# Performance work log

Measured on AMD Instinct MI355X. Metric: run time of the kernel, lower is better.

Reference implementation:

```python
import jax, jax.numpy as jnp
import numpy as np

NHEAD = 8

def setup_inputs() -> dict:
    key = jax.random.key(0)
    ks = jax.random.split(key, 6)
    b, n, d = 4, 1024, 512
    emb = jax.random.normal(ks[0], (b, n, d), dtype=jnp.float32)
    dirs = jax.random.normal(ks[1], (b, n, n, 3), dtype=jnp.float32)
    d_mask = jax.random.normal(ks[2], (b * NHEAD, n, n), dtype=jnp.float32) * 0.1
    W_proj = jax.random.normal(ks[3], (d, 3 * d), dtype=jnp.float32) / np.sqrt(d)
    b_proj = jnp.zeros((3 * d,), dtype=jnp.float32)
    w_force = jax.random.normal(ks[4], (d,), dtype=jnp.float32) / np.sqrt(d)
    b_force = jnp.zeros((1,), dtype=jnp.float32)
    return {"emb": emb, "dirs": dirs, "d_mask": d_mask, "W_proj": W_proj,
            "b_proj": b_proj, "w_force": w_force, "b_force": b_force}

def reference(emb, dirs, d_mask, W_proj, b_proj, w_force, b_force):
    b, n, d = emb.shape
    h = NHEAD
    dh = d // h
    scale = jnp.asarray(np.sqrt(d), emb.dtype)
    qkv = emb @ W_proj + b_proj                      # (b,n,3d)
    q, k, v = jnp.split(qkv, 3, axis=-1)
    q = q.reshape(b, n, h, dh).transpose(0, 2, 1, 3) / scale   # (b,h,n,dh)
    k = k.reshape(b, n, h, dh).transpose(0, 2, 1, 3)           # (b,h,n,dh)
    v = v.reshape(b, n, h, dh).transpose(0, 2, 1, 3)           # (b,h,n,dh)
    scores = jnp.einsum('bhid,bhjd->bhij', q, k) + d_mask.reshape(b, h, n, n)
    attn = jax.nn.softmax(scores, axis=-1)                     # (b,h,n,n); dropout in eval mode = identity
    # torch: (attn[...,None] * dirs[:,None]) @ v  materializes (b,h,n,n,3);
    # fused einsum computes the same per-axis weighted sum without it.
    xyz = jnp.einsum('bhij,bija,bhjd->biahd', attn, dirs, v)   # (b,n,3,h,dh)
    xyz = xyz.reshape(b, n, 3, d)
    out = jnp.einsum('bnad,d->bna', xyz, w_force) + b_force[0]  # (b,n,3)
    return out
```

## Files before the change

kernel.cpp:

```cpp
#include <hip/hip_runtime.h>
#include <hip/hip_bf16.h>

#define NH 8
#define BB 4
#define NN 1024
#define DD 512
#define DH 64
#define JSPLIT 4

typedef __bf16 bf16x8 __attribute__((ext_vector_type(8)));
typedef float f32x4 __attribute__((ext_vector_type(4)));

__device__ __forceinline__ unsigned short f2bf(float f) {
    union { float f; unsigned u; } v; v.f = f;
    unsigned u = v.u;
    unsigned r = u + 0x7FFFu + ((u >> 16) & 1u);
    return (unsigned short)(r >> 16);
}

__global__ void k_wv(const float* __restrict__ W, const float* __restrict__ w_force,
                     const float* __restrict__ b_proj, float* __restrict__ wv_eff,
                     float* __restrict__ s_bias) {
    int t = blockIdx.x * blockDim.x + threadIdx.x;
    int c = t >> 3, h = t & 7;
    float acc = 0.f;
    for (int dh = 0; dh < DH; ++dh)
        acc += W[c * (3 * DD) + 2 * DD + h * DH + dh] * w_force[h * DH + dh];
    wv_eff[c * 8 + h] = acc;
    if (t < 8) {
        float sb = 0.f;
        for (int dh = 0; dh < DH; ++dh)
            sb += b_proj[2 * DD + t * DH + dh] * w_force[t * DH + dh];
        s_bias[t] = sb;
    }
}

__global__ void k_wt(const float* __restrict__ W, const float* __restrict__ b_proj,
                     unsigned short* __restrict__ Wt, float* __restrict__ bias_eff) {
    __shared__ float tile[32][33];
    int c0 = blockIdx.x * 32;
    int n0 = blockIdx.y * 32;
    int t = threadIdx.x;
    for (int i = 0; i < 4; ++i) {
        int idx = t + i * 256;
        int r = idx >> 5, cn = idx & 31;
        tile[r][cn] = W[(c0 + r) * (3 * DD) + n0 + cn];
    }
    __syncthreads();
    const float rscale = 0.044194173824159216f;
    for (int i = 0; i < 4; ++i) {
        int idx = t + i * 256;
        int nn = idx >> 5, cc = idx & 31;
        float v = tile[cc][nn];
        int n = n0 + nn;
        if (n < DD) v *= rscale;
        Wt[n * DD + c0 + cc] = f2bf(v);
    }
    if (blockIdx.x == 0 && t < 32) {
        int n = n0 + t;
        bias_eff[n] = b_proj[n] * (n < DD ? 0.044194173824159216f : 1.0f);
    }
}

__global__ void k_emb(const float* __restrict__ emb, unsigned short* __restrict__ embb) {
    int t = blockIdx.x * blockDim.x + threadIdx.x;
    float4 v = ((const float4*)emb)[t];
    ushort4 o;
    o.x = f2bf(v.x); o.y = f2bf(v.y); o.z = f2bf(v.z); o.w = f2bf(v.w);
    ((ushort4*)embb)[t] = o;
}

__global__ __launch_bounds__(256) void k_s(const float* __restrict__ emb,
                                           const float* __restrict__ wv_eff,
                                           const float* __restrict__ s_bias,
                                           float* __restrict__ s_ws) {
    __shared__ float wv[DD * 8];
    int t = threadIdx.x;
    for (int i = 0; i < 16; ++i) wv[t + i * 256] = wv_eff[t + i * 256];
    __syncthreads();
    int wave = t >> 6, lane = t & 63;
    int row = blockIdx.x * 4 + wave;
    int c0 = lane * 8;
    float partial[8] = {0, 0, 0, 0, 0, 0, 0, 0};
    const float* er = emb + row * DD + c0;
    #pragma unroll
    for (int e = 0; e < 8; ++e) {
        float v = er[e];
        const float* wr = &wv[(c0 + e) * 8];
        #pragma unroll
        for (int h = 0; h < 8; ++h) partial[h] += v * wr[h];
    }
    float val = 0.f;
    #pragma unroll
    for (int h = 0; h < 8; ++h) {
        float p = partial[h];
        for (int off = 32; off; off >>= 1) p += __shfl_xor(p, off);
        if (lane == h) val = p;
    }
    if (lane < 8) {
        int b = row >> 10, j = row & 1023;
        s_ws[(b * 8 + lane) * NN + j] = val + s_bias[lane];
    }
}

__global__ __launch_bounds__(256) void k_gemm(const unsigned short* __restrict__ embb,
                                              const unsigned short* __restrict__ Wt,
                                              const float* __restrict__ bias_eff,
                                              unsigned short* __restrict__ qb,
                                              unsigned short* __restrict__ kb) {
    __shared__ __align__(16) unsigned short a_s[64 * 40];
    __shared__ __align__(16) unsigned short b_s[64 * 40];
    int m0 = blockIdx.x * 64, n0 = blockIdx.y * 64;
    int t = threadIdx.x;
    int wave = t >> 6, lane = t & 63;
    int wr = (wave >> 1) * 32, wc = (wave & 1) * 32;
    int qd = lane >> 4, l16 = lane & 15;
    int sr = t >> 2, sg = (t & 3) * 8;
    f32x4 acc[2][2] = {};
    for (int k0 = 0; k0 < DD; k0 += 32) {
        uint4 av = *(const uint4*)(embb + (m0 + sr) * DD + k0 + sg);
        uint4 bv = *(const uint4*)(Wt + (n0 + sr) * DD + k0 + sg);
        __syncthreads();
        *(uint4*)(&a_s[sr * 40 + sg]) = av;
        *(uint4*)(&b_s[sr * 40 + sg]) = bv;
        __syncthreads();
        bf16x8 af0 = *(const bf16x8*)(&a_s[(wr + l16) * 40 + qd * 8]);
        bf16x8 af1 = *(const bf16x8*)(&a_s[(wr + 16 + l16) * 40 + qd * 8]);
        bf16x8 bf0 = *(const bf16x8*)(&b_s[(wc + l16) * 40 + qd * 8]);
        bf16x8 bf1 = *(const bf16x8*)(&b_s[(wc + 16 + l16) * 40 + qd * 8]);
        acc[0][0] = __builtin_amdgcn_mfma_f32_16x16x32_bf16(af0, bf0, acc[0][0], 0, 0, 0);
        acc[0][1] = __builtin_amdgcn_mfma_f32_16x16x32_bf16(af0, bf1, acc[0][1], 0, 0, 0);
        acc[1][0] = __builtin_amdgcn_mfma_f32_16x16x32_bf16(af1, bf0, acc[1][0], 0, 0, 0);
        acc[1][1] = __builtin_amdgcn_mfma_f32_16x16x32_bf16(af1, bf1, acc[1][1], 0, 0, 0);
    }
    #pragma unroll
    for (int mi = 0; mi < 2; ++mi)
        #pragma unroll
        for (int ni = 0; ni < 2; ++ni) {
            int col = n0 + wc + ni * 16 + l16;
            float be = bias_eff[col];
            #pragma unroll
            for (int r = 0; r < 4; ++r) {
                int row = m0 + wr + mi * 16 + qd * 4 + r;
                unsigned short bvv = f2bf(acc[mi][ni][r] + be);
                if (col < DD) qb[row * DD + col] = bvv;
                else          kb[row * DD + col - DD] = bvv;
            }
        }
}

__global__ __launch_bounds__(512) void k_attn(const unsigned short* __restrict__ qb,
                                              const unsigned short* __restrict__ kb,
                                              const float* __restrict__ s_ws,
                                              const float* __restrict__ d_mask,
                                              const float* __restrict__ dirs,
                                              float4* __restrict__ part) {
    int blk = blockIdx.x;
    int itile = blk & 63;
    int bc = blk >> 6;
    int b = bc & 3;
    int chunk = bc >> 2;
    int i0 = itile * 16;
    int j_base = chunk * (NN / JSPLIT);
    int t = threadIdx.x;
    int h = t >> 6, lane = t & 63;
    int qd = lane >> 4, c = lane & 15;
    int i = i0 + c;

    const unsigned short* qbase = qb + ((b * NN + i) * DD + h * DH + qd * 8);
    bf16x8 aq0 = *(const bf16x8*)(qbase);
    bf16x8 aq1 = *(const bf16x8*)(qbase + 32);

    float acc0 = 0.f, acc1 = 0.f, acc2 = 0.f, l = 0.f;
    const float* sm   = s_ws + (b * NH + h) * NN;
    const float* mrow = d_mask + (size_t)(b * NH + h) * NN * NN + (size_t)i * NN;
    const float* drow = dirs + ((size_t)b * NN + i) * NN * 3;

    for (int j0 = j_base; j0 < j_base + NN / JSPLIT; j0 += 16) {
        const unsigned short* kba = kb + ((b * NN + j0 + c) * DD + h * DH + qd * 8);
        bf16x8 bk0 = *(const bf16x8*)(kba);
        bf16x8 bk1 = *(const bf16x8*)(kba + 32);
        f32x4 sc = {0.f, 0.f, 0.f, 0.f};
        sc = __builtin_amdgcn_mfma_f32_16x16x32_bf16(bk0, aq0, sc, 0, 0, 0);
        sc = __builtin_amdgcn_mfma_f32_16x16x32_bf16(bk1, aq1, sc, 0, 0, 0);
        int jq = j0 + qd * 4;
        float4 mk = *(const float4*)(mrow + jq);
        float4 sj = *(const float4*)(sm + jq);
        float4 d0 = *(const float4*)(drow + jq * 3);
        float4 d1 = *(const float4*)(drow + jq * 3 + 4);
        float4 d2 = *(const float4*)(drow + jq * 3 + 8);
        float p0 = __expf(sc[0] + mk.x);
        float p1 = __expf(sc[1] + mk.y);
        float p2 = __expf(sc[2] + mk.z);
        float p3 = __expf(sc[3] + mk.w);
        l += p0 + p1 + p2 + p3;
        float t0 = p0 * sj.x, t1 = p1 * sj.y, t2 = p2 * sj.z, t3 = p3 * sj.w;
        acc0 += t0 * d0.x + t1 * d0.w + t2 * d1.z + t3 * d2.y;
        acc1 += t0 * d0.y + t1 * d1.x + t2 * d1.w + t3 * d2.z;
        acc2 += t0 * d0.z + t1 * d1.y + t2 * d2.x + t3 * d2.w;
    }
    l    += __shfl_xor(l, 16);    l    += __shfl_xor(l, 32);
    acc0 += __shfl_xor(acc0, 16); acc0 += __shfl_xor(acc0, 32);
    acc1 += __shfl_xor(acc1, 16); acc1 += __shfl_xor(acc1, 32);
    acc2 += __shfl_xor(acc2, 16); acc2 += __shfl_xor(acc2, 32);
    if (qd == 0) {
        float4 o; o.x = l; o.y = acc0; o.z = acc1; o.w = acc2;
        part[((size_t)bc * NH + h) * NN + i] = o;
    }
}

__global__ __launch_bounds__(256) void k_fin(const float4* __restrict__ part,
                                             const float* __restrict__ b_force,
                                             float* __restrict__ out) {
    int t = blockIdx.x * 256 + threadIdx.x;
    int b = t >> 10, i = t & 1023;
    float o0, o1, o2;
    o0 = o1 = o2 = b_force[0];
    #pragma unroll
    for (int h = 0; h < NH; ++h) {
        float lx = 0.f, a0 = 0.f, a1 = 0.f, a2 = 0.f;
        #pragma unroll
        for (int ch = 0; ch < JSPLIT; ++ch) {
            float4 p = part[(((size_t)(ch * BB + b) * NH + h) * NN) + i];
            lx += p.x; a0 += p.y; a1 += p.z; a2 += p.w;
        }
        float inv = 1.0f / lx;
        o0 += a0 * inv; o1 += a1 * inv; o2 += a2 * inv;
    }
    out[t * 3 + 0] = o0;
    out[t * 3 + 1] = o1;
    out[t * 3 + 2] = o2;
}

extern "C" void kernel_launch(void* const* d_in, const int* in_sizes, int n_in,
                              void* d_out, int out_size, void* d_ws, size_t ws_size,
                              hipStream_t stream) {
    (void)in_sizes; (void)n_in; (void)out_size; (void)ws_size;
    const float* emb     = (const float*)d_in[0];
    const float* dirs    = (const float*)d_in[1];
    const float* d_mask  = (const float*)d_in[2];
    const float* W       = (const float*)d_in[3];
    const float* b_proj  = (const float*)d_in[4];
    const float* w_force = (const float*)d_in[5];
    const float* b_force = (const float*)d_in[6];
    float* out = (float*)d_out;

    char* ws = (char*)d_ws;
    float* wv_eff   = (float*)ws;
    float* s_bias   = wv_eff + 4096;
    float* bias_eff = s_bias + 8;
    float* s_ws     = bias_eff + 1024;
    unsigned short* Wt   = (unsigned short*)(s_ws + 32768);
    unsigned short* embb = Wt + 1024 * 512;
    unsigned short* qb   = embb + 4096 * 512;
    unsigned short* kb   = qb + 4096 * 512;
    float4* part = (float4*)(kb + 4096 * 512);

    hipLaunchKernelGGL(k_wv,   dim3(16),      dim3(256), 0, stream, W, w_force, b_proj, wv_eff, s_bias);
    hipLaunchKernelGGL(k_wt,   dim3(16, 32),  dim3(256), 0, stream, W, b_proj, Wt, bias_eff);
    hipLaunchKernelGGL(k_emb,  dim3(2048),    dim3(256), 0, stream, emb, embb);
    hipLaunchKernelGGL(k_s,    dim3(1024),    dim3(256), 0, stream, emb, wv_eff, s_bias, s_ws);
    hipLaunchKernelGGL(k_gemm, dim3(64, 16),  dim3(256), 0, stream, embb, Wt, bias_eff, qb, kb);
    hipLaunchKernelGGL(k_attn, dim3(BB * 64 * JSPLIT), dim3(512), 0, stream,
                       qb, kb, s_ws, d_mask, dirs, part);
    hipLaunchKernelGGL(k_fin,  dim3(16),      dim3(256), 0, stream, part, b_force, out);
}
```

Baseline: 351.4 us.

## Prefetch attention loads, split heads across blocks, enlarge GEMM tiles, parallelise reductions

The attention kernel splits each block's eight heads into two 256-thread blocks and software-pipelines the K, mask, s and dirs loads one step ahead, with nontemporal loads for the mask. The QK projection GEMM moves to 128x128 tiles with a 4x4 MFMA tile per wave and no LDS padding. The wv and s precompute kernels are restructured for more parallelism and coalesced access. The head split may double dirs reads, and the unpadded LDS layout can cause bank conflicts.

```diff
diff --git a/kernel.cpp b/kernel.cpp
--- a/kernel.cpp
+++ b/kernel.cpp
@@ -18,20 +18,27 @@
     return (unsigned short)(r >> 16);
 }
 
-__global__ void k_wv(const float* __restrict__ W, const float* __restrict__ w_force,
-                     const float* __restrict__ b_proj, float* __restrict__ wv_eff,
-                     float* __restrict__ s_bias) {
-    int t = blockIdx.x * blockDim.x + threadIdx.x;
-    int c = t >> 3, h = t & 7;
-    float acc = 0.f;
-    for (int dh = 0; dh < DH; ++dh)
-        acc += W[c * (3 * DD) + 2 * DD + h * DH + dh] * w_force[h * DH + dh];
-    wv_eff[c * 8 + h] = acc;
-    if (t < 8) {
-        float sb = 0.f;
-        for (int dh = 0; dh < DH; ++dh)
-            sb += b_proj[2 * DD + t * DH + dh] * w_force[t * DH + dh];
-        s_bias[t] = sb;
+__global__ __launch_bounds__(256) void k_wv(const float* __restrict__ W, const float* __restrict__ w_force,
+                                            const float* __restrict__ b_proj, float* __restrict__ wv_eff,
+                                            float* __restrict__ s_bias) {
+    int wave = threadIdx.x >> 6, lane = threadIdx.x & 63;
+    if (blockIdx.x == 128) {
+        if (wave == 0) {
+            for (int hh = 0; hh < NH; ++hh) {
+                float p = b_proj[2 * DD + hh * DH + lane] * w_force[hh * DH + lane];
+                for (int off = 32; off; off >>= 1) p += __shfl_xor(p, off);
+                if (lane == 0) s_bias[hh] = p;
+            }
+        }
+        return;
+    }
+    int c = blockIdx.x * 4 + wave;
+    const float* wr = W + (size_t)c * (3 * DD) + 2 * DD;
+    #pragma unroll
+    for (int hh = 0; hh < NH; ++hh) {
+        float p = wr[hh * DH + lane] * w_force[hh * DH + lane];
+        for (int off = 32; off; off >>= 1) p += __shfl_xor(p, off);
+        if (lane == 0) wv_eff[c * 8 + hh] = p;
     }
 }
 
@@ -74,33 +81,22 @@
                                            const float* __restrict__ wv_eff,
                                            const float* __restrict__ s_bias,
                                            float* __restrict__ s_ws) {
-    __shared__ float wv[DD * 8];
-    int t = threadIdx.x;
-    for (int i = 0; i < 16; ++i) wv[t + i * 256] = wv_eff[t + i * 256];
-    __syncthreads();
-    int wave = t >> 6, lane = t & 63;
-    int row = blockIdx.x * 4 + wave;
-    int c0 = lane * 8;
-    float partial[8] = {0, 0, 0, 0, 0, 0, 0, 0};
-    const float* er = emb + row * DD + c0;
-    #pragma unroll
-    for (int e = 0; e < 8; ++e) {
-        float v = er[e];
-        const float* wr = &wv[(c0 + e) * 8];
-        #pragma unroll
-        for (int h = 0; h < 8; ++h) partial[h] += v * wr[h];
-    }
-    float val = 0.f;
-    #pragma unroll
-    for (int h = 0; h < 8; ++h) {
-        float p = partial[h];
-        for (int off = 32; off; off >>= 1) p += __shfl_xor(p, off);
-        if (lane == h) val = p;
-    }
-    if (lane < 8) {
-        int b = row >> 10, j = row & 1023;
-        s_ws[(b * 8 + lane) * NN + j] = val + s_bias[lane];
-    }
+    int t = blockIdx.x * 256 + threadIdx.x;
+    int row = t >> 3;
+    int h = t & 7;
+    const float* er = emb + (size_t)row * DD;
+    const float* wp = wv_eff + h;
+    float acc = 0.f;
+    #pragma unroll 8
+    for (int c4 = 0; c4 < DD / 4; ++c4) {
+        float4 e = *(const float4*)(er + c4 * 4);
+        acc += e.x * wp[(c4 * 4 + 0) * 8];
+        acc += e.y * wp[(c4 * 4 + 1) * 8];
+        acc += e.z * wp[(c4 * 4 + 2) * 8];
+        acc += e.w * wp[(c4 * 4 + 3) * 8];
+    }
+    int b = row >> 10, j = row & 1023;
+    s_ws[(b * 8 + h) * NN + j] = acc + s_bias[h];
 }
 
 __global__ __launch_bounds__(256) void k_gemm(const unsigned short* __restrict__ embb,
@@ -108,87 +104,98 @@
                                               const float* __restrict__ bias_eff,
                                               unsigned short* __restrict__ qb,
                                               unsigned short* __restrict__ kb) {
-    __shared__ __align__(16) unsigned short a_s[64 * 40];
-    __shared__ __align__(16) unsigned short b_s[64 * 40];
-    int m0 = blockIdx.x * 64, n0 = blockIdx.y * 64;
+    __shared__ __align__(16) unsigned short a_s[128 * 32];
+    __shared__ __align__(16) unsigned short b_s[128 * 32];
+    int m0 = blockIdx.x * 128, n0 = blockIdx.y * 128;
     int t = threadIdx.x;
     int wave = t >> 6, lane = t & 63;
-    int wr = (wave >> 1) * 32, wc = (wave & 1) * 32;
-    int qd = lane >> 4, l16 = lane & 15;
+    int wr = (wave >> 1) * 64, wc = (wave & 1) * 64;
+    int qd = lane >> 4, c = lane & 15;
     int sr = t >> 2, sg = (t & 3) * 8;
-    f32x4 acc[2][2] = {};
+    f32x4 acc[4][4] = {};
     for (int k0 = 0; k0 < DD; k0 += 32) {
-        uint4 av = *(const uint4*)(embb + (m0 + sr) * DD + k0 + sg);
-        uint4 bv = *(const uint4*)(Wt + (n0 + sr) * DD + k0 + sg);
+        uint4 av0 = *(const uint4*)(embb + (size_t)(m0 + sr) * DD + k0 + sg);
+        uint4 av1 = *(const uint4*)(embb + (size_t)(m0 + 64 + sr) * DD + k0 + sg);
+        uint4 bv0 = *(const uint4*)(Wt + (size_t)(n0 + sr) * DD + k0 + sg);
+        uint4 bv1 = *(const uint4*)(Wt + (size_t)(n0 + 64 + sr) * DD + k0 + sg);
         __syncthreads();
-        *(uint4*)(&a_s[sr * 40 + sg]) = av;
-        *(uint4*)(&b_s[sr * 40 + sg]) = bv;
+        *(uint4*)(&a_s[sr * 32 + sg]) = av0;
+        *(uint4*)(&a_s[(64 + sr) * 32 + sg]) = av1;
+        *(uint4*)(&b_s[sr * 32 + sg]) = bv0;
+        *(uint4*)(&b_s[(64 + sr) * 32 + sg]) = bv1;
         __syncthreads();
-        bf16x8 af0 = *(const bf16x8*)(&a_s[(wr + l16) * 40 + qd * 8]);
-        bf16x8 af1 = *(const bf16x8*)(&a_s[(wr + 16 + l16) * 40 + qd * 8]);
-        bf16x8 bf0 = *(const bf16x8*)(&b_s[(wc + l16) * 40 + qd * 8]);
-        bf16x8 bf1 = *(const bf16x8*)(&b_s[(wc + 16 + l16) * 40 + qd * 8]);
-        acc[0][0] = __builtin_amdgcn_mfma_f32_16x16x32_bf16(af0, bf0, acc[0][0], 0, 0, 0);
-        acc[0][1] = __builtin_amdgcn_mfma_f32_16x16x32_bf16(af0, bf1, acc[0][1], 0, 0, 0);
-        acc[1][0] = __builtin_amdgcn_mfma_f32_16x16x32_bf16(af1, bf0, acc[1][0], 0, 0, 0);
-        acc[1][1] = __builtin_amdgcn_mfma_f32_16x16x32_bf16(af1, bf1, acc[1][1], 0, 0, 0);
-    }
-    #pragma unroll
-    for (int mi = 0; mi < 2; ++mi)
-        #pragma unroll
-        for (int ni = 0; ni < 2; ++ni) {
-            int col = n0 + wc + ni * 16 + l16;
-            float be = bias_eff[col];
+        bf16x8 af[4], bfr[4];
+        #pragma unroll
+        for (int mi = 0; mi < 4; ++mi)
+            af[mi] = *(const bf16x8*)(&a_s[(wr + mi * 16 + c) * 32 + qd * 8]);
+        #pragma unroll
+        for (int ni = 0; ni < 4; ++ni)
+            bfr[ni] = *(const bf16x8*)(&b_s[(wc + ni * 16 + c) * 32 + qd * 8]);
+        #pragma unroll
+        for (int mi = 0; mi < 4; ++mi)
+            #pragma unroll
+            for (int ni = 0; ni < 4; ++ni)
+                acc[mi][ni] = __builtin_amdgcn_mfma_f32_16x16x32_bf16(af[mi], bfr[ni], acc[mi][ni], 0, 0, 0);
+    }
+    bool isQ = (n0 < DD);
+    unsigned short* dst = isQ ? qb : kb;
+    int nb = isQ ? n0 : n0 - DD;
+    #pragma unroll
+    for (int mi = 0; mi < 4; ++mi)
+        #pragma unroll
+        for (int ni = 0; ni < 4; ++ni) {
+            int col = nb + wc + ni * 16 + c;
+            float be = bias_eff[isQ ? col : col + DD];
             #pragma unroll
             for (int r = 0; r < 4; ++r) {
                 int row = m0 + wr + mi * 16 + qd * 4 + r;
-                unsigned short bvv = f2bf(acc[mi][ni][r] + be);
-                if (col < DD) qb[row * DD + col] = bvv;
-                else          kb[row * DD + col - DD] = bvv;
+                dst[(size_t)row * DD + col] = f2bf(acc[mi][ni][r] + be);
             }
         }
 }
 
-__global__ __launch_bounds__(512) void k_attn(const unsigned short* __restrict__ qb,
+__global__ __launch_bounds__(256) void k_attn(const unsigned short* __restrict__ qb,
                                               const unsigned short* __restrict__ kb,
                                               const float* __restrict__ s_ws,
                                               const float* __restrict__ d_mask,
                                               const float* __restrict__ dirs,
-                                              float4* __restrict__ part) {
+                                              float* __restrict__ part) {
     int blk = blockIdx.x;
     int itile = blk & 63;
-    int bc = blk >> 6;
-    int b = bc & 3;
-    int chunk = bc >> 2;
+    int rest = blk >> 6;
+    int hg = rest & 1;
+    int b = (rest >> 1) & 3;
+    int chunk = rest >> 3;
     int i0 = itile * 16;
     int j_base = chunk * (NN / JSPLIT);
     int t = threadIdx.x;
-    int h = t >> 6, lane = t & 63;
-    int qd = lane >> 4, c = lane & 15;
+    int h = hg * 4 + (t >> 6);
+    int lane = t & 63, qd = lane >> 4, c = lane & 15;
     int i = i0 + c;
 
-    const unsigned short* qbase = qb + ((b * NN + i) * DD + h * DH + qd * 8);
+    const unsigned short* qbase = qb + ((size_t)(b * NN + i) * DD + h * DH + qd * 8);
     bf16x8 aq0 = *(const bf16x8*)(qbase);
     bf16x8 aq1 = *(const bf16x8*)(qbase + 32);
 
+    const unsigned short* kp = kb + ((size_t)(b * NN + j_base + c) * DD + h * DH + qd * 8);
+    const float* mp = d_mask + (size_t)(b * NH + h) * NN * NN + (size_t)i * NN + j_base + qd * 4;
+    const float* sp = s_ws + (b * NH + h) * NN + j_base + qd * 4;
+    const float* dp = dirs + (((size_t)b * NN + i) * NN + j_base + qd * 4) * 3;
+
     float acc0 = 0.f, acc1 = 0.f, acc2 = 0.f, l = 0.f;
-    const float* sm   = s_ws + (b * NH + h) * NN;
-    const float* mrow = d_mask + (size_t)(b * NH + h) * NN * NN + (size_t)i * NN;
-    const float* drow = dirs + ((size_t)b * NN + i) * NN * 3;
-
-    for (int j0 = j_base; j0 < j_base + NN / JSPLIT; j0 += 16) {
-        const unsigned short* kba = kb + ((b * NN + j0 + c) * DD + h * DH + qd * 8);
-        bf16x8 bk0 = *(const bf16x8*)(kba);
-        bf16x8 bk1 = *(const bf16x8*)(kba + 32);
+
+    bf16x8 ck0 = *(const bf16x8*)(kp);
+    bf16x8 ck1 = *(const bf16x8*)(kp + 32);
+    f32x4 cmk = __builtin_nontemporal_load((const f32x4*)mp);
+    f32x4 csj = *(const f32x4*)sp;
+    f32x4 cd0 = *(const f32x4*)(dp);
+    f32x4 cd1 = *(const f32x4*)(dp + 4);
+    f32x4 cd2 = *(const f32x4*)(dp + 8);
+
+    auto step = [&](bf16x8 k0, bf16x8 k1, f32x4 mk, f32x4 sj, f32x4 d0, f32x4 d1, f32x4 d2) {
         f32x4 sc = {0.f, 0.f, 0.f, 0.f};
-        sc = __builtin_amdgcn_mfma_f32_16x16x32_bf16(bk0, aq0, sc, 0, 0, 0);
-        sc = __builtin_amdgcn_mfma_f32_16x16x32_bf16(bk1, aq1, sc, 0, 0, 0);
-        int jq = j0 + qd * 4;
-        float4 mk = *(const float4*)(mrow + jq);
-        float4 sj = *(const float4*)(sm + jq);
-        float4 d0 = *(const float4*)(drow + jq * 3);
-        float4 d1 = *(const float4*)(drow + jq * 3 + 4);
-        float4 d2 = *(const float4*)(drow + jq * 3 + 8);
+        sc = __builtin_amdgcn_mfma_f32_16x16x32_bf16(k0, aq0, sc, 0, 0, 0);
+        sc = __builtin_amdgcn_mfma_f32_16x16x32_bf16(k1, aq1, sc, 0, 0, 0);
         float p0 = __expf(sc[0] + mk.x);
         float p1 = __expf(sc[1] + mk.y);
         float p2 = __expf(sc[2] + mk.z);
@@ -198,14 +205,30 @@
         acc0 += t0 * d0.x + t1 * d0.w + t2 * d1.z + t3 * d2.y;
         acc1 += t0 * d0.y + t1 * d1.x + t2 * d1.w + t3 * d2.z;
         acc2 += t0 * d0.z + t1 * d1.y + t2 * d2.x + t3 * d2.w;
-    }
+    };
+
+    #pragma unroll
+    for (int it = 0; it < NN / JSPLIT / 16 - 1; ++it) {
+        kp += 16 * DD; mp += 16; sp += 16; dp += 48;
+        bf16x8 nk0 = *(const bf16x8*)(kp);
+        bf16x8 nk1 = *(const bf16x8*)(kp + 32);
+        f32x4 nmk = __builtin_nontemporal_load((const f32x4*)mp);
+        f32x4 nsj = *(const f32x4*)sp;
+        f32x4 nd0 = *(const f32x4*)(dp);
+        f32x4 nd1 = *(const f32x4*)(dp + 4);
+        f32x4 nd2 = *(const f32x4*)(dp + 8);
+        step(ck0, ck1, cmk, csj, cd0, cd1, cd2);
+        ck0 = nk0; ck1 = nk1; cmk = nmk; csj = nsj; cd0 = nd0; cd1 = nd1; cd2 = nd2;
+    }
+    step(ck0, ck1, cmk, csj, cd0, cd1, cd2);
+
     l    += __shfl_xor(l, 16);    l    += __shfl_xor(l, 32);
     acc0 += __shfl_xor(acc0, 16); acc0 += __shfl_xor(acc0, 32);
     acc1 += __shfl_xor(acc1, 16); acc1 += __shfl_xor(acc1, 32);
     acc2 += __shfl_xor(acc2, 16); acc2 += __shfl_xor(acc2, 32);
     if (qd == 0) {
-        float4 o; o.x = l; o.y = acc0; o.z = acc1; o.w = acc2;
-        part[((size_t)bc * NH + h) * NN + i] = o;
+        f32x4 o; o[0] = l; o[1] = acc0; o[2] = acc1; o[3] = acc2;
+        *(f32x4*)(part + ((((size_t)(chunk * BB + b)) * NH + h) * NN + i) * 4) = o;
     }
 }
 
@@ -254,14 +277,14 @@
     unsigned short* embb = Wt + 1024 * 512;
     unsigned short* qb   = embb + 4096 * 512;
     unsigned short* kb   = qb + 4096 * 512;
-    float4* part = (float4*)(kb + 4096 * 512);
-
-    hipLaunchKernelGGL(k_wv,   dim3(16),      dim3(256), 0, stream, W, w_force, b_proj, wv_eff, s_bias);
+    float* part = (float*)(kb + 4096 * 512);
+
+    hipLaunchKernelGGL(k_wv,   dim3(129),     dim3(256), 0, stream, W, w_force, b_proj, wv_eff, s_bias);
     hipLaunchKernelGGL(k_wt,   dim3(16, 32),  dim3(256), 0, stream, W, b_proj, Wt, bias_eff);
     hipLaunchKernelGGL(k_emb,  dim3(2048),    dim3(256), 0, stream, emb, embb);
-    hipLaunchKernelGGL(k_s,    dim3(1024),    dim3(256), 0, stream, emb, wv_eff, s_bias, s_ws);
-    hipLaunchKernelGGL(k_gemm, dim3(64, 16),  dim3(256), 0, stream, embb, Wt, bias_eff, qb, kb);
-    hipLaunchKernelGGL(k_attn, dim3(BB * 64 * JSPLIT), dim3(512), 0, stream,
+    hipLaunchKernelGGL(k_s,    dim3(128),     dim3(256), 0, stream, emb, wv_eff, s_bias, s_ws);
+    hipLaunchKernelGGL(k_gemm, dim3(32, 8),   dim3(256), 0, stream, embb, Wt, bias_eff, qb, kb);
+    hipLaunchKernelGGL(k_attn, dim3(BB * 64 * JSPLIT * 2), dim3(256), 0, stream,
                        qb, kb, s_ws, d_mask, dirs, part);
-    hipLaunchKernelGGL(k_fin,  dim3(16),      dim3(256), 0, stream, part, b_force, out);
-}
+    hipLaunchKernelGGL(k_fin,  dim3(16),      dim3(256), 0, stream, (const float4*)part, b_force, out);
+}
```

After: 344.0 us. -2.1%, faster.
